# Kernel tuning notes

Measured on AMD Instinct MI355X. Metric: run time of the kernel, lower is better.

Reference implementation:

```python
import jax, jax.numpy as jnp
import numpy as np

# Grid parameters (from init_kwargs)
GRID_W, GRID_L, GRID_H = 96, 96, 48
VOXEL_SIZE = 0.05
MIN_POINTS_PER_VOXEL = 10


def setup_inputs() -> dict:
    key = jax.random.key(0)
    k1, k2 = jax.random.split(key, 2)
    # points uniform over a ~[0,1.5]^3 sub-volume so voxel occupancy is realistic
    point_coordinates = jax.random.uniform(k1, (4, 3, 480, 640), jnp.float32) * 1.5
    point_attributes = jax.random.normal(k2, (4, 16, 480, 640), jnp.float32)
    origin = jnp.zeros((4, 3), jnp.float32)
    return {"point_coordinates": point_coordinates,
            "point_attributes": point_attributes,
            "origin": origin}


def _voxelize_one(coords, attrs, org):
    # coords: [3, N], attrs: [C, N], org: [3]
    V = GRID_W * GRID_L * GRID_H
    bounds = jnp.array([GRID_W, GRID_L, GRID_H], jnp.int32)
    # per-point voxel index (floor == .long() for positive; OOB handled by mask)
    idx3 = jnp.floor((coords - org[:, None]) / VOXEL_SIZE).astype(jnp.int32)  # [3, N]
    in_bounds = jnp.all((idx3 >= 0) & (idx3 < bounds[:, None]), axis=0)       # [N]
    flat = idx3[0] * (GRID_L * GRID_H) + idx3[1] * GRID_H + idx3[2]           # [N]
    flat = jnp.where(in_bounds, flat, 0)  # route OOB points to voxel 0, masked out
    # occupancy: scatter-add of in-bounds mask
    counts = jax.ops.segment_sum(in_bounds.astype(jnp.float32), flat, num_segments=V)
    # max-pool of attributes per voxel; OOB points contribute -inf
    masked = jnp.where(in_bounds[None, :], attrs, -jnp.inf)                   # [C, N]
    vmax = jax.ops.segment_max(masked.T, flat, num_segments=V).T              # [C, V]
    occ = counts >= MIN_POINTS_PER_VOXEL                                      # [V]
    data = jnp.where(occ[None, :] & jnp.isfinite(vmax), vmax, 0.0)            # [C, V]
    return data, occ


def reference(point_coordinates, point_attributes, origin):
    b, c = point_attributes.shape[:2]
    coords = point_coordinates.reshape(b, 3, -1)   # [B, 3, N]
    attrs = point_attributes.reshape(b, c, -1)     # [B, C, N]
    data, occ = jax.vmap(_voxelize_one)(coords, attrs, origin)
    voxeldata = data.reshape(b, c, GRID_W, GRID_L, GRID_H)
    voxeloccupancy = occ.reshape(b, 1, GRID_W, GRID_L, GRID_H).astype(jnp.float32)
    return voxeldata, voxeloccupancy
```

## Files before the change

### kernel.cpp

```cpp
#include <hip/hip_runtime.h>
#include <cstdint>
#include <math.h>

#define GRID_W 96
#define GRID_L 96
#define GRID_H 48
#define NVOX (GRID_W * GRID_L * GRID_H)
#define VOXEL_SIZE 0.05f
#define MIN_PTS 10
#define BATCH 4
#define CHANS 16
#define NPTS (480 * 640)
#define TOTPTS (BATCH * NPTS)
#define TOTVOX (BATCH * NVOX)

#define SCAN_BLKS 864
#define SCAN_TPB 256
#define SCAN_EPT 8
#define SCAN_CHUNK (SCAN_TPB * SCAN_EPT)

#define ROWW 8

typedef unsigned nt_uint4  __attribute__((ext_vector_type(4)));
typedef float    nt_float4 __attribute__((ext_vector_type(4)));
typedef float    nt_float2 __attribute__((ext_vector_type(2)));

#define WS_OFFSETS 0
#define WS_VR      ((TOTVOX + 4) * 4)
#define WS_IDS     (WS_VR + TOTPTS * 4)
#define WS_ROWS    (WS_IDS + TOTPTS * 4 + 16)
#define WS_SUMS    (WS_ROWS + (size_t)TOTPTS * ROWW * 4)
#define WS_NEEDED  ((size_t)(WS_SUMS + 4096))

__device__ __forceinline__ unsigned bf16_rtne(float f) {
    unsigned u = __float_as_uint(f);
    return (u + 0x7FFFu + ((u >> 16) & 1u)) >> 16;
}
__device__ __forceinline__ unsigned pack2(float lo, float hi) {
    return bf16_rtne(lo) | (bf16_rtne(hi) << 16);
}


__global__ void k_hist_pack(const float* __restrict__ coords,
                            const float* __restrict__ attrs,
                            const float* __restrict__ origin,
                            unsigned*    __restrict__ vr,
                            unsigned*    __restrict__ rows,
                            unsigned*    __restrict__ cnt)
{
    int t = blockIdx.x * blockDim.x + threadIdx.x;
    if (t >= TOTPTS / 2) return;
    int pid = t * 2;
    int b = pid / NPTS;
    int n = pid - b * NPTS;

    const float* cb = coords + (size_t)b * 3 * NPTS;
    nt_float2 X = __builtin_nontemporal_load((const nt_float2*)(cb + n));
    nt_float2 Y = __builtin_nontemporal_load((const nt_float2*)(cb + NPTS + n));
    nt_float2 Z = __builtin_nontemporal_load((const nt_float2*)(cb + 2 * NPTS + n));
    float ox = origin[b * 3 + 0];
    float oy = origin[b * 3 + 1];
    float oz = origin[b * 3 + 2];

    const float* ab = attrs + (size_t)b * CHANS * NPTS + n;
    unsigned w[2][ROWW];
    #pragma unroll
    for (int c = 0; c < CHANS; c += 2) {
        nt_float2 a0 = __builtin_nontemporal_load((const nt_float2*)(ab + (size_t)c * NPTS));
        nt_float2 a1 = __builtin_nontemporal_load((const nt_float2*)(ab + (size_t)(c + 1) * NPTS));
        w[0][c >> 1] = pack2(a0.x, a1.x);
        w[1][c >> 1] = pack2(a0.y, a1.y);
    }
    uint4* dst = (uint4*)(rows + (size_t)pid * ROWW);
    dst[0] = uint4{w[0][0], w[0][1], w[0][2], w[0][3]};
    dst[1] = uint4{w[0][4], w[0][5], w[0][6], w[0][7]};
    dst[2] = uint4{w[1][0], w[1][1], w[1][2], w[1][3]};
    dst[3] = uint4{w[1][4], w[1][5], w[1][6], w[1][7]};

    float xs[2] = {X.x, X.y};
    float ys[2] = {Y.x, Y.y};
    float zs[2] = {Z.x, Z.y};
    unsigned ps[2];
    #pragma unroll
    for (int k = 0; k < 2; ++k) {
        int ix = (int)floorf((xs[k] - ox) / VOXEL_SIZE);
        int iy = (int)floorf((ys[k] - oy) / VOXEL_SIZE);
        int iz = (int)floorf((zs[k] - oz) / VOXEL_SIZE);
        unsigned p = 0xFFFFFFFFu;
        if ((unsigned)ix < GRID_W && (unsigned)iy < GRID_L && (unsigned)iz < GRID_H) {
            int v = b * NVOX + ix * (GRID_L * GRID_H) + iy * GRID_H + iz;
            unsigned r = atomicAdd(&cnt[v], 1u);
            p = ((unsigned)v << 10) | (r & 1023u);
        }
        ps[k] = p;
    }
    *(uint2*)(vr + pid) = uint2{ps[0], ps[1]};
}

__global__ void k_scan1(unsigned* __restrict__ offsets,
                        unsigned* __restrict__ sums,
                        float*    __restrict__ occ)
{
    __shared__ unsigned s[SCAN_TPB];
    int t = threadIdx.x;
    int base = blockIdx.x * SCAN_CHUNK + t * SCAN_EPT;

    uint4 a = ((const uint4*)(offsets + base))[0];
    uint4 c = ((const uint4*)(offsets + base))[1];
    unsigned e[SCAN_EPT] = {a.x, a.y, a.z, a.w, c.x, c.y, c.z, c.w};

    nt_float4 oc0, oc1;
    oc0.x = (e[0] >= MIN_PTS) ? 1.f : 0.f;  oc0.y = (e[1] >= MIN_PTS) ? 1.f : 0.f;
    oc0.z = (e[2] >= MIN_PTS) ? 1.f : 0.f;  oc0.w = (e[3] >= MIN_PTS) ? 1.f : 0.f;
    oc1.x = (e[4] >= MIN_PTS) ? 1.f : 0.f;  oc1.y = (e[5] >= MIN_PTS) ? 1.f : 0.f;
    oc1.z = (e[6] >= MIN_PTS) ? 1.f : 0.f;  oc1.w = (e[7] >= MIN_PTS) ? 1.f : 0.f;
    __builtin_nontemporal_store(oc0, ((nt_float4*)(occ + base)));
    __builtin_nontemporal_store(oc1, ((nt_float4*)(occ + base)) + 1);

    unsigned tot = 0;
    #pragma unroll
    for (int k = 0; k < SCAN_EPT; ++k) { unsigned v = e[k]; e[k] = tot; tot += v; }

    s[t] = tot;
    __syncthreads();
    #pragma unroll
    for (int off = 1; off < SCAN_TPB; off <<= 1) {
        unsigned v = (t >= off) ? s[t - off] : 0u;
        __syncthreads();
        s[t] += v;
        __syncthreads();
    }
    unsigned prefix = s[t] - tot;
    #pragma unroll
    for (int k = 0; k < SCAN_EPT; ++k) e[k] += prefix;

    ((uint4*)(offsets + base))[0] = uint4{e[0], e[1], e[2], e[3]};
    ((uint4*)(offsets + base))[1] = uint4{e[4], e[5], e[6], e[7]};

    if (t == SCAN_TPB - 1) sums[blockIdx.x] = s[t];
}

__global__ void k_scan2(unsigned* __restrict__ sums) {
    __shared__ unsigned s[1024];
    int t = threadIdx.x;
    unsigned my = (t < SCAN_BLKS) ? sums[t] : 0u;
    s[t] = my;
    __syncthreads();
    #pragma unroll
    for (int off = 1; off < 1024; off <<= 1) {
        unsigned v = (t >= off) ? s[t - off] : 0u;
        __syncthreads();
        s[t] += v;
        __syncthreads();
    }
    if (t < SCAN_BLKS) sums[t] = s[t] - my;
    if (t == SCAN_BLKS - 1) sums[SCAN_BLKS] = s[t];
}

__global__ void k_scatter_ids4(const unsigned* __restrict__ vr,
                               const unsigned* __restrict__ offsets,
                               const unsigned* __restrict__ sums,
                               int*            __restrict__ ids)
{
    int t = blockIdx.x * blockDim.x + threadIdx.x;
    if (t >= TOTPTS / 4) return;
    int pid = t * 4;
    uint4 P = *(const uint4*)(vr + pid);
    unsigned ps[4] = {P.x, P.y, P.z, P.w};
    #pragma unroll
    for (int k = 0; k < 4; ++k) {
        if (ps[k] != 0xFFFFFFFFu) {
            unsigned v = ps[k] >> 10;
            unsigned pos = offsets[v] + sums[v >> 11] + (ps[k] & 1023u);
            ids[pos] = pid + k;
        }
    }
}

__global__ void k_gather_ind2(const unsigned* __restrict__ rows,
                              const int*      __restrict__ ids,
                              const unsigned* __restrict__ offsets,
                              const unsigned* __restrict__ sums,
                              float*          __restrict__ data)
{
    int g = blockIdx.x * blockDim.x + threadIdx.x;
    if (g >= TOTVOX / 2) return;
    int vox0 = g * 2;

    uint2 O = *(const uint2*)(offsets + vox0);
    unsigned base = sums[vox0 >> 11];
    unsigned s[3];
    s[0] = O.x + base;
    s[1] = O.y + base;
    s[2] = offsets[vox0 + 2] + sums[(vox0 + 2) >> 11];

    float m[2][CHANS];
    #pragma unroll
    for (int q = 0; q < 2; ++q) {
        unsigned k = s[q + 1] - s[q];
        unsigned s0 = s[q];
        if (k >= MIN_PTS) {
            const float ninf = -__builtin_inff();
            #pragma unroll
            for (int c = 0; c < CHANS; ++c) m[q][c] = ninf;
            unsigned j = 0;
            for (; j + 2 <= k; j += 2) {
                int p0 = ids[s0 + j];
                int p1 = ids[s0 + j + 1];
                const uint4* r0p = (const uint4*)(rows + (size_t)p0 * ROWW);
                const uint4* r1p = (const uint4*)(rows + (size_t)p1 * ROWW);
                uint4 l0 = r0p[0], h0 = r0p[1];
                uint4 l1 = r1p[0], h1 = r1p[1];
                unsigned wa[8] = {l0.x, l0.y, l0.z, l0.w, h0.x, h0.y, h0.z, h0.w};
                unsigned wb[8] = {l1.x, l1.y, l1.z, l1.w, h1.x, h1.y, h1.z, h1.w};
                #pragma unroll
                for (int h = 0; h < 8; ++h) {
                    m[q][2 * h]     = fmaxf(m[q][2 * h],
                                        fmaxf(__uint_as_float(wa[h] << 16),
                                              __uint_as_float(wb[h] << 16)));
                    m[q][2 * h + 1] = fmaxf(m[q][2 * h + 1],
                                        fmaxf(__uint_as_float(wa[h] & 0xFFFF0000u),
                                              __uint_as_float(wb[h] & 0xFFFF0000u)));
                }
            }
            if (j < k) {
                int p0 = ids[s0 + j];
                const uint4* r0p = (const uint4*)(rows + (size_t)p0 * ROWW);
                uint4 l0 = r0p[0], h0 = r0p[1];
                unsigned wa[8] = {l0.x, l0.y, l0.z, l0.w, h0.x, h0.y, h0.z, h0.w};
                #pragma unroll
                for (int h = 0; h < 8; ++h) {
                    m[q][2 * h]     = fmaxf(m[q][2 * h], __uint_as_float(wa[h] << 16));
                    m[q][2 * h + 1] = fmaxf(m[q][2 * h + 1],
                                            __uint_as_float(wa[h] & 0xFFFF0000u));
                }
            }
            #pragma unroll
            for (int c = 0; c < CHANS; ++c) if (!isfinite(m[q][c])) m[q][c] = 0.f;
        } else {
            #pragma unroll
            for (int c = 0; c < CHANS; ++c) m[q][c] = 0.f;
        }
    }

    int b = vox0 / NVOX;
    int v0 = vox0 - b * NVOX;
    float* db = data + (size_t)b * CHANS * NVOX + v0;
    #pragma unroll
    for (int c = 0; c < CHANS; ++c) {
        nt_float2 o = {m[0][c], m[1][c]};
        __builtin_nontemporal_store(o, (nt_float2*)(db + (size_t)c * NVOX));
    }
}


__device__ __forceinline__ unsigned flip_f32(float f) {
    unsigned u = __float_as_uint(f);
    unsigned mask = (unsigned)(-(int)(u >> 31)) | 0x80000000u;
    return u ^ mask;
}
__device__ __forceinline__ float unflip_f32(unsigned u) {
    unsigned mask = ((u >> 31) - 1u) | 0x80000000u;
    return __uint_as_float(u ^ mask);
}
#define FLIP_NEG_INF 0x007FFFFFu

__global__ void pv_init(uint4* __restrict__ out) {
    const int DATA4 = BATCH * CHANS * NVOX / 4;
    const int TOT4  = BATCH * (CHANS + 1) * NVOX / 4;
    int i = blockIdx.x * blockDim.x + threadIdx.x;
    if (i < TOT4) {
        unsigned val = (i < DATA4) ? FLIP_NEG_INF : 0u;
        out[i] = uint4{val, val, val, val};
    }
}

__global__ void pv_scatter(const float* __restrict__ coords,
                           const float* __restrict__ attrs,
                           const float* __restrict__ origin,
                           unsigned*    __restrict__ data_u,
                           unsigned*    __restrict__ cnt)
{
    int id = blockIdx.x * blockDim.x + threadIdx.x;
    if (id >= TOTPTS) return;
    int b = id / NPTS;
    int n = id - b * NPTS;
    const float* cb = coords + (size_t)b * 3 * NPTS;
    float x = cb[n], y = cb[NPTS + n], z = cb[2 * NPTS + n];
    float ox = origin[b * 3 + 0], oy = origin[b * 3 + 1], oz = origin[b * 3 + 2];
    int ix = (int)floorf((x - ox) / VOXEL_SIZE);
    int iy = (int)floorf((y - oy) / VOXEL_SIZE);
    int iz = (int)floorf((z - oz) / VOXEL_SIZE);
    if ((unsigned)ix < GRID_W && (unsigned)iy < GRID_L && (unsigned)iz < GRID_H) {
        int flat = ix * (GRID_L * GRID_H) + iy * GRID_H + iz;
        atomicAdd(&cnt[b * NVOX + flat], 1u);
        const float* ab = attrs + (size_t)b * CHANS * NPTS + n;
        unsigned*    db = data_u + (size_t)b * CHANS * NVOX + flat;
        #pragma unroll
        for (int c = 0; c < CHANS; ++c)
            atomicMax(&db[(size_t)c * NVOX], flip_f32(ab[(size_t)c * NPTS]));
    }
}

__global__ void pv_finalize(unsigned* __restrict__ data_u,
                            unsigned* __restrict__ cnt_u)
{
    int id = blockIdx.x * blockDim.x + threadIdx.x;
    if (id >= TOTVOX) return;
    int b = id / NVOX;
    int v = id - b * NVOX;
    unsigned cnt = cnt_u[id];
    bool occ = (cnt >= MIN_PTS);
    ((float*)cnt_u)[id] = occ ? 1.0f : 0.0f;
    unsigned* db = data_u + (size_t)b * CHANS * NVOX + v;
    #pragma unroll
    for (int c = 0; c < CHANS; ++c) {
        float f = unflip_f32(db[(size_t)c * NVOX]);
        ((float*)db)[(size_t)c * NVOX] = (occ && isfinite(f)) ? f : 0.0f;
    }
}


extern "C" void kernel_launch(void* const* d_in, const int* in_sizes, int n_in,
                              void* d_out, int out_size, void* d_ws, size_t ws_size,
                              hipStream_t stream) {
    const float* coords = (const float*)d_in[0];
    const float* attrs  = (const float*)d_in[1];
    const float* origin = (const float*)d_in[2];

    float* out = (float*)d_out;
    float* data = out;
    float* occ  = out + (size_t)BATCH * CHANS * NVOX;

    if (ws_size >= WS_NEEDED) {
        char* ws = (char*)d_ws;
        unsigned* offsets = (unsigned*)(ws + WS_OFFSETS);
        unsigned* vr      = (unsigned*)(ws + WS_VR);
        int*      ids     = (int*)(ws + WS_IDS);
        unsigned* rows    = (unsigned*)(ws + WS_ROWS);
        unsigned* sums    = (unsigned*)(ws + WS_SUMS);

        (void)hipMemsetAsync(offsets, 0, (size_t)(TOTVOX + 4) * 4, stream);
        k_hist_pack<<<(TOTPTS / 2 + 255) / 256, 256, 0, stream>>>(coords, attrs, origin,
                                                                  vr, rows, offsets);
        k_scan1<<<SCAN_BLKS, SCAN_TPB, 0, stream>>>(offsets, sums, occ);
        k_scan2<<<1, 1024, 0, stream>>>(sums);
        k_scatter_ids4<<<(TOTPTS / 4 + 255) / 256, 256, 0, stream>>>(vr, offsets, sums, ids);
        k_gather_ind2<<<(TOTVOX / 2 + 255) / 256, 256, 0, stream>>>(rows, ids, offsets, sums, data);
    } else {
        unsigned* data_u = (unsigned*)data;
        unsigned* cnt    = (unsigned*)occ;
        const int TOT4 = BATCH * (CHANS + 1) * NVOX / 4;
        pv_init<<<(TOT4 + 255) / 256, 256, 0, stream>>>((uint4*)d_out);
        pv_scatter<<<(TOTPTS + 255) / 256, 256, 0, stream>>>(coords, attrs, origin, data_u, cnt);
        pv_finalize<<<(TOTVOX + 255) / 256, 256, 0, stream>>>(data_u, cnt);
    }
}
```

Baseline: 285.9 us.

## Gather only occupied voxels via worklist and zero output during scan

The scan kernel now zero-fills the voxel data output and builds a compact worklist of occupied voxels with an atomic counter. The gather kernel becomes a grid-stride loop over that worklist instead of visiting every voxel. Most voxels are empty, so this aims to avoid launching threads and reading offsets for them, and to spread the uneven gather work across more threads. In exchange it adds a contended global atomic in the scan and scattered, uncoalesced stores in the gather. The hist kernel also moves its attribute packing after the atomic binning.

```diff
diff --git a/kernel.cpp b/kernel.cpp
--- a/kernel.cpp
+++ b/kernel.cpp
@@ -18,6 +18,7 @@
 #define SCAN_TPB 256
 #define SCAN_EPT 8
 #define SCAN_CHUNK (SCAN_TPB * SCAN_EPT)
+#define CHUNKS_PER_BATCH (NVOX / SCAN_CHUNK)
 
 #define ROWW 8
 
@@ -30,7 +31,8 @@
 #define WS_IDS     (WS_VR + TOTPTS * 4)
 #define WS_ROWS    (WS_IDS + TOTPTS * 4 + 16)
 #define WS_SUMS    (WS_ROWS + (size_t)TOTPTS * ROWW * 4)
-#define WS_NEEDED  ((size_t)(WS_SUMS + 4096))
+#define WS_WORK    (WS_SUMS + 8192)
+#define WS_NEEDED  ((size_t)(WS_WORK + (size_t)TOTVOX * 4 + 4096))
 
 __device__ __forceinline__ unsigned bf16_rtne(float f) {
     unsigned u = __float_as_uint(f);
@@ -61,21 +63,6 @@
     float ox = origin[b * 3 + 0];
     float oy = origin[b * 3 + 1];
     float oz = origin[b * 3 + 2];
-
-    const float* ab = attrs + (size_t)b * CHANS * NPTS + n;
-    unsigned w[2][ROWW];
-    #pragma unroll
-    for (int c = 0; c < CHANS; c += 2) {
-        nt_float2 a0 = __builtin_nontemporal_load((const nt_float2*)(ab + (size_t)c * NPTS));
-        nt_float2 a1 = __builtin_nontemporal_load((const nt_float2*)(ab + (size_t)(c + 1) * NPTS));
-        w[0][c >> 1] = pack2(a0.x, a1.x);
-        w[1][c >> 1] = pack2(a0.y, a1.y);
-    }
-    uint4* dst = (uint4*)(rows + (size_t)pid * ROWW);
-    dst[0] = uint4{w[0][0], w[0][1], w[0][2], w[0][3]};
-    dst[1] = uint4{w[0][4], w[0][5], w[0][6], w[0][7]};
-    dst[2] = uint4{w[1][0], w[1][1], w[1][2], w[1][3]};
-    dst[3] = uint4{w[1][4], w[1][5], w[1][6], w[1][7]};
 
     float xs[2] = {X.x, X.y};
     float ys[2] = {Y.x, Y.y};
@@ -94,12 +81,31 @@
         }
         ps[k] = p;
     }
+
+    const float* ab = attrs + (size_t)b * CHANS * NPTS + n;
+    unsigned w[2][ROWW];
+    #pragma unroll
+    for (int c = 0; c < CHANS; c += 2) {
+        nt_float2 a0 = __builtin_nontemporal_load((const nt_float2*)(ab + (size_t)c * NPTS));
+        nt_float2 a1 = __builtin_nontemporal_load((const nt_float2*)(ab + (size_t)(c + 1) * NPTS));
+        w[0][c >> 1] = pack2(a0.x, a1.x);
+        w[1][c >> 1] = pack2(a0.y, a1.y);
+    }
+    uint4* dst = (uint4*)(rows + (size_t)pid * ROWW);
+    dst[0] = uint4{w[0][0], w[0][1], w[0][2], w[0][3]};
+    dst[1] = uint4{w[0][4], w[0][5], w[0][6], w[0][7]};
+    dst[2] = uint4{w[1][0], w[1][1], w[1][2], w[1][3]};
+    dst[3] = uint4{w[1][4], w[1][5], w[1][6], w[1][7]};
+
     *(uint2*)(vr + pid) = uint2{ps[0], ps[1]};
 }
 
 __global__ void k_scan1(unsigned* __restrict__ offsets,
                         unsigned* __restrict__ sums,
-                        float*    __restrict__ occ)
+                        float*    __restrict__ occ,
+                        float*    __restrict__ data,
+                        int*      __restrict__ worklist,
+                        unsigned* __restrict__ nocc)
 {
     __shared__ unsigned s[SCAN_TPB];
     int t = threadIdx.x;
@@ -117,6 +123,27 @@
     __builtin_nontemporal_store(oc0, ((nt_float4*)(occ + base)));
     __builtin_nontemporal_store(oc1, ((nt_float4*)(occ + base)) + 1);
 
+    #pragma unroll
+    for (int k = 0; k < SCAN_EPT; ++k) {
+        if (e[k] >= MIN_PTS) {
+            unsigned wp = atomicAdd(nocc, 1u);
+            worklist[wp] = base + k;
+        }
+    }
+
+    {
+        int bb   = blockIdx.x / CHUNKS_PER_BATCH;
+        int vloc = (blockIdx.x % CHUNKS_PER_BATCH) * SCAN_CHUNK + t * SCAN_EPT;
+        float* dz = data + (size_t)bb * CHANS * NVOX + vloc;
+        nt_float4 z4 = {0.f, 0.f, 0.f, 0.f};
+        #pragma unroll
+        for (int cc = 0; cc < CHANS; ++cc) {
+            nt_float4* p = (nt_float4*)(dz + (size_t)cc * NVOX);
+            __builtin_nontemporal_store(z4, p);
+            __builtin_nontemporal_store(z4, p + 1);
+        }
+    }
+
     unsigned tot = 0;
     #pragma unroll
     for (int k = 0; k < SCAN_EPT; ++k) { unsigned v = e[k]; e[k] = tot; tot += v; }
@@ -177,79 +204,66 @@
     }
 }
 
-__global__ void k_gather_ind2(const unsigned* __restrict__ rows,
-                              const int*      __restrict__ ids,
-                              const unsigned* __restrict__ offsets,
-                              const unsigned* __restrict__ sums,
-                              float*          __restrict__ data)
-{
-    int g = blockIdx.x * blockDim.x + threadIdx.x;
-    if (g >= TOTVOX / 2) return;
-    int vox0 = g * 2;
-
-    uint2 O = *(const uint2*)(offsets + vox0);
-    unsigned base = sums[vox0 >> 11];
-    unsigned s[3];
-    s[0] = O.x + base;
-    s[1] = O.y + base;
-    s[2] = offsets[vox0 + 2] + sums[(vox0 + 2) >> 11];
-
-    float m[2][CHANS];
-    #pragma unroll
-    for (int q = 0; q < 2; ++q) {
-        unsigned k = s[q + 1] - s[q];
-        unsigned s0 = s[q];
-        if (k >= MIN_PTS) {
-            const float ninf = -__builtin_inff();
+__global__ void k_gather_occ(const unsigned* __restrict__ rows,
+                             const int*      __restrict__ ids,
+                             const unsigned* __restrict__ offsets,
+                             const unsigned* __restrict__ sums,
+                             const int*      __restrict__ worklist,
+                             const unsigned* __restrict__ nocc,
+                             float*          __restrict__ data)
+{
+    unsigned nw = *nocc;
+    unsigned stride = gridDim.x * blockDim.x;
+    for (unsigned i = blockIdx.x * blockDim.x + threadIdx.x; i < nw; i += stride) {
+        int vox = worklist[i];
+        unsigned s0 = offsets[vox] + sums[vox >> 11];
+        unsigned s1 = offsets[vox + 1] + sums[(vox + 1) >> 11];
+        unsigned k = s1 - s0;
+
+        const float ninf = -__builtin_inff();
+        float m[CHANS];
+        #pragma unroll
+        for (int c = 0; c < CHANS; ++c) m[c] = ninf;
+
+        unsigned j = 0;
+        for (; j + 2 <= k; j += 2) {
+            int p0 = ids[s0 + j];
+            int p1 = ids[s0 + j + 1];
+            const uint4* r0p = (const uint4*)(rows + (size_t)p0 * ROWW);
+            const uint4* r1p = (const uint4*)(rows + (size_t)p1 * ROWW);
+            uint4 l0 = r0p[0], h0 = r0p[1];
+            uint4 l1 = r1p[0], h1 = r1p[1];
+            unsigned wa[8] = {l0.x, l0.y, l0.z, l0.w, h0.x, h0.y, h0.z, h0.w};
+            unsigned wb[8] = {l1.x, l1.y, l1.z, l1.w, h1.x, h1.y, h1.z, h1.w};
             #pragma unroll
-            for (int c = 0; c < CHANS; ++c) m[q][c] = ninf;
-            unsigned j = 0;
-            for (; j + 2 <= k; j += 2) {
-                int p0 = ids[s0 + j];
-                int p1 = ids[s0 + j + 1];
-                const uint4* r0p = (const uint4*)(rows + (size_t)p0 * ROWW);
-                const uint4* r1p = (const uint4*)(rows + (size_t)p1 * ROWW);
-                uint4 l0 = r0p[0], h0 = r0p[1];
-                uint4 l1 = r1p[0], h1 = r1p[1];
-                unsigned wa[8] = {l0.x, l0.y, l0.z, l0.w, h0.x, h0.y, h0.z, h0.w};
-                unsigned wb[8] = {l1.x, l1.y, l1.z, l1.w, h1.x, h1.y, h1.z, h1.w};
-                #pragma unroll
-                for (int h = 0; h < 8; ++h) {
-                    m[q][2 * h]     = fmaxf(m[q][2 * h],
-                                        fmaxf(__uint_as_float(wa[h] << 16),
-                                              __uint_as_float(wb[h] << 16)));
-                    m[q][2 * h + 1] = fmaxf(m[q][2 * h + 1],
-                                        fmaxf(__uint_as_float(wa[h] & 0xFFFF0000u),
-                                              __uint_as_float(wb[h] & 0xFFFF0000u)));
-                }
+            for (int h = 0; h < 8; ++h) {
+                m[2 * h]     = fmaxf(m[2 * h],
+                                 fmaxf(__uint_as_float(wa[h] << 16),
+                                       __uint_as_float(wb[h] << 16)));
+                m[2 * h + 1] = fmaxf(m[2 * h + 1],
+                                 fmaxf(__uint_as_float(wa[h] & 0xFFFF0000u),
+                                       __uint_as_float(wb[h] & 0xFFFF0000u)));
             }
-            if (j < k) {
-                int p0 = ids[s0 + j];
-                const uint4* r0p = (const uint4*)(rows + (size_t)p0 * ROWW);
-                uint4 l0 = r0p[0], h0 = r0p[1];
-                unsigned wa[8] = {l0.x, l0.y, l0.z, l0.w, h0.x, h0.y, h0.z, h0.w};
-                #pragma unroll
-                for (int h = 0; h < 8; ++h) {
-                    m[q][2 * h]     = fmaxf(m[q][2 * h], __uint_as_float(wa[h] << 16));
-                    m[q][2 * h + 1] = fmaxf(m[q][2 * h + 1],
-                                            __uint_as_float(wa[h] & 0xFFFF0000u));
-                }
+        }
+        if (j < k) {
+            int p0 = ids[s0 + j];
+            const uint4* r0p = (const uint4*)(rows + (size_t)p0 * ROWW);
+            uint4 l0 = r0p[0], h0 = r0p[1];
+            unsigned wa[8] = {l0.x, l0.y, l0.z, l0.w, h0.x, h0.y, h0.z, h0.w};
+            #pragma unroll
+            for (int h = 0; h < 8; ++h) {
+                m[2 * h]     = fmaxf(m[2 * h], __uint_as_float(wa[h] << 16));
+                m[2 * h + 1] = fmaxf(m[2 * h + 1], __uint_as_float(wa[h] & 0xFFFF0000u));
             }
-            #pragma unroll
-            for (int c = 0; c < CHANS; ++c) if (!isfinite(m[q][c])) m[q][c] = 0.f;
-        } else {
-            #pragma unroll
-            for (int c = 0; c < CHANS; ++c) m[q][c] = 0.f;
-        }
-    }
-
-    int b = vox0 / NVOX;
-    int v0 = vox0 - b * NVOX;
-    float* db = data + (size_t)b * CHANS * NVOX + v0;
-    #pragma unroll
-    for (int c = 0; c < CHANS; ++c) {
-        nt_float2 o = {m[0][c], m[1][c]};
-        __builtin_nontemporal_store(o, (nt_float2*)(db + (size_t)c * NVOX));
+        }
+        #pragma unroll
+        for (int c = 0; c < CHANS; ++c) if (!isfinite(m[c])) m[c] = 0.f;
+
+        int b = vox / NVOX;
+        int v = vox - b * NVOX;
+        float* db = data + (size_t)b * CHANS * NVOX + v;
+        #pragma unroll
+        for (int c = 0; c < CHANS; ++c) db[(size_t)c * NVOX] = m[c];
     }
 }
 
@@ -339,14 +353,16 @@
         int*      ids     = (int*)(ws + WS_IDS);
         unsigned* rows    = (unsigned*)(ws + WS_ROWS);
         unsigned* sums    = (unsigned*)(ws + WS_SUMS);
+        int*      work    = (int*)(ws + WS_WORK);
+        unsigned* nocc    = offsets + TOTVOX + 2;
 
         (void)hipMemsetAsync(offsets, 0, (size_t)(TOTVOX + 4) * 4, stream);
         k_hist_pack<<<(TOTPTS / 2 + 255) / 256, 256, 0, stream>>>(coords, attrs, origin,
                                                                   vr, rows, offsets);
-        k_scan1<<<SCAN_BLKS, SCAN_TPB, 0, stream>>>(offsets, sums, occ);
+        k_scan1<<<SCAN_BLKS, SCAN_TPB, 0, stream>>>(offsets, sums, occ, data, work, nocc);
         k_scan2<<<1, 1024, 0, stream>>>(sums);
         k_scatter_ids4<<<(TOTPTS / 4 + 255) / 256, 256, 0, stream>>>(vr, offsets, sums, ids);
-        k_gather_ind2<<<(TOTVOX / 2 + 255) / 256, 256, 0, stream>>>(rows, ids, offsets, sums, data);
+        k_gather_occ<<<1024, 256, 0, stream>>>(rows, ids, offsets, sums, work, nocc, data);
     } else {
         unsigned* data_u = (unsigned*)data;
         unsigned* cnt    = (unsigned*)occ;
```

New measurement: 342.7 us. 19.8% more time.
